# Optimization experiments

Measured on AMD Instinct MI355X. Metric: run time of the kernel, lower is better.

## Reference

```python
import jax, jax.numpy as jnp
import numpy as np

N, M, E, IN, HID = 100000, 2048, 65536, 512, 256
TAU, LAMDA = 0.5, 1.0


def _l2n(a, eps=1e-12):
    # F.normalize: x / max(||x||_2, eps) along dim=1
    return a / jnp.maximum(jnp.linalg.norm(a, axis=1, keepdims=True), eps)


def setup_inputs() -> dict:
    key = jax.random.key(0)
    ks = jax.random.split(key, 16)
    s = 0.05  # weight scale (xavier-like)
    inp = {
        "x": jax.random.normal(ks[0], (N, IN), jnp.float32),
        "We0": jax.random.normal(ks[1], (IN, HID), jnp.float32) * s,
        "be0": jnp.zeros((HID,), jnp.float32),
        "We1": jax.random.normal(ks[2], (HID, HID), jnp.float32) * s,
        "be1": jnp.zeros((HID,), jnp.float32),
        "Wt0": jax.random.normal(ks[3], (IN, HID), jnp.float32) * s,
        "bt0": jnp.zeros((HID,), jnp.float32),
        "Wt1": jax.random.normal(ks[4], (HID, HID), jnp.float32) * s,
        "bt1": jnp.zeros((HID,), jnp.float32),
        "Wp0": jax.random.normal(ks[5], (HID, HID), jnp.float32) * s,
        "bp0": jnp.zeros((HID,), jnp.float32),
        "Wp1": jax.random.normal(ks[6], (HID, HID), jnp.float32) * s,
        "bp1": jnp.zeros((HID,), jnp.float32),
        "p_vals": jnp.ones((N,), jnp.float32),
        "cg_vals": jax.random.uniform(ks[7], (E,), jnp.float32),
        "p_assign": jax.random.randint(ks[8], (N,), 0, M, jnp.int32),
        "cg_rows": jax.random.randint(ks[9], (E,), 0, M, jnp.int32),
        "cg_cols": jax.random.randint(ks[10], (E,), 0, M, jnp.int32),
        "neg_idx": jax.random.randint(ks[11], (N,), 0, M, jnp.int32),
    }
    return inp


def reference(x, We0, be0, We1, be1, Wt0, bt0, Wt1, bt1,
              Wp0, bp0, Wp1, bp1, p_vals, cg_vals,
              p_assign, cg_rows, cg_cols, neg_idx):
    # encoder: stacked Linears, no activation (batch_norm=layer_norm=False)
    h = (x @ We0 + be0) @ We1 + be1                      # [N, HID]
    # h = spmm(P.T, h): per-cluster weighted sum
    hc = jax.ops.segment_sum(p_vals[:, None] * h, p_assign, num_segments=M)  # [M, HID]
    # target encoder
    v = (x @ Wt0 + bt0) @ Wt1 + bt1                      # [N, HID]

    # pos_score: projector (relu between layers, none on last) + normalize
    q = jax.nn.relu(hc @ Wp0 + bp0) @ Wp1 + bp1          # [M, HID]
    q = _l2n(q)
    vn = _l2n(v)
    pos_sim = jnp.sum(vn * q[p_assign], axis=1) / TAU    # [N]
    pos_score = jnp.exp(
        jax.ops.segment_sum(p_vals * pos_sim, p_assign, num_segments=M))[:, None]  # [M,1]

    # neg_score: dense cluster-cluster similarity
    hn = _l2n(hc)
    neg_score = jnp.exp((hn @ hn.T) / TAU)               # [M, M]

    # partition_score = coarse_g @ neg_score (sparse row-scatter)
    partition_score = jax.ops.segment_sum(
        cg_vals[:, None] * neg_score[cg_cols], cg_rows, num_segments=M)  # [M, M]

    loss = jnp.mean(-jnp.log(pos_score + LAMDA * partition_score)
                    + jnp.log(pos_score + neg_score.sum(axis=1)))
    return loss
```

## Files before the change

kernel.cpp:

```cpp
#include <hip/hip_runtime.h>
#include <hip/hip_bf16.h>
#include <math.h>

#define N_PTS  100000
#define M_CL   2048
#define E_EDG  65536
#define IN_DIM 512
#define HID    256

typedef unsigned short u16;
typedef __attribute__((ext_vector_type(8))) short bf16x8;
typedef __attribute__((ext_vector_type(4))) float f32x4;

__device__ __forceinline__ u16 f2bf(float f){
  __hip_bfloat16 h = __float2bfloat16(f);
  return *reinterpret_cast<u16*>(&h);
}
__device__ __forceinline__ unsigned pk2(float a, float b){
  return (unsigned)f2bf(a) | ((unsigned)f2bf(b) << 16);
}
__device__ __forceinline__ float bf2f(u16 v){
  return __uint_as_float((unsigned)v << 16);
}
__device__ __forceinline__ void glds16(const u16* g, u16* lds_base_uniform){
  __builtin_amdgcn_global_load_lds(
      (const __attribute__((address_space(1))) unsigned int*)(g),
      (__attribute__((address_space(3))) unsigned int*)(lds_base_uniform), 16, 0, 0);
}
#define VMWAIT8() do{ asm volatile("s_waitcnt vmcnt(8)" ::: "memory"); __builtin_amdgcn_sched_barrier(0);}while(0)
#define VMWAIT4() do{ asm volatile("s_waitcnt vmcnt(4)" ::: "memory"); __builtin_amdgcn_sched_barrier(0);}while(0)
#define VMWAIT0() do{ asm volatile("s_waitcnt vmcnt(0)" ::: "memory"); __builtin_amdgcn_sched_barrier(0);}while(0)

static const size_t OFF_POSACC = 0;
static const size_t OFF_NEGSUM = 8192;
static const size_t OFF_HISTP  = 16384;
static const size_t OFF_CURP   = 24576;
static const size_t OFF_HISTE  = 32768;
static const size_t OFF_CURE   = 40960;
static const size_t OFF_LOSS   = 49152;
static const size_t ZERO_BYTES = 49408;
static const size_t OFF_STARTP = 49664;
static const size_t OFF_STARTE = 58112;
static const size_t OFF_SORTPT = 66560;
static const size_t OFF_SCOL   = 466688;
static const size_t OFF_SVAL   = 728832;
static const size_t OFF_CNT    = 990976;
static const size_t OFF_XC     = 999168;
static const size_t OFF_Q      = 9387776;
static const size_t OFF_HNB    = 11484928;
static const size_t OFF_NEGB   = 13582080;
static const size_t OFF_WT0T   = 22020096;
static const size_t OFF_WT1T   = 22282240;
static const size_t OFF_XBF    = 33554432;

__global__ __launch_bounds__(256) void k_zero(unsigned* __restrict__ p, int n){
  int i = blockIdx.x*256 + threadIdx.x;
  if (i < n) p[i] = 0u;
}

__global__ __launch_bounds__(256) void k_hist(const int* __restrict__ idx, int n, int* __restrict__ hist){
  int i = blockIdx.x*256 + threadIdx.x;
  if (i < n) atomicAdd(&hist[idx[i]], 1);
}

__global__ __launch_bounds__(256) void k_scan(const int* __restrict__ hist, int* __restrict__ start){
  __shared__ int part[256];
  int t = threadIdx.x;
  int v[8]; int s = 0;
#pragma unroll
  for (int j=0;j<8;j++){ v[j] = hist[t*8+j]; s += v[j]; }
  part[t] = s;
  __syncthreads();
  if (t == 0){
    int run = 0;
    for (int i=0;i<256;i++){ int tmp = part[i]; part[i] = run; run += tmp; }
  }
  __syncthreads();
  int run = part[t];
#pragma unroll
  for (int j=0;j<8;j++){ start[t*8+j] = run; run += v[j]; }
  if (t == 255) start[M_CL] = run;
}

__global__ __launch_bounds__(256) void k_scatter_pts(const int* __restrict__ assign, const int* __restrict__ start,
                                                     int* __restrict__ cur, int* __restrict__ out){
  int i = blockIdx.x*256 + threadIdx.x;
  if (i < N_PTS){
    int r = assign[i];
    int p = start[r] + atomicAdd(&cur[r], 1);
    out[p] = i;
  }
}

__global__ __launch_bounds__(256) void k_scatter_edges(const int* __restrict__ rows, const int* __restrict__ cols,
                                                       const float* __restrict__ vals, const int* __restrict__ start,
                                                       int* __restrict__ cur, int* __restrict__ scol,
                                                       float* __restrict__ sval){
  int e = blockIdx.x*256 + threadIdx.x;
  if (e < E_EDG){
    int r = rows[e];
    int p = start[r] + atomicAdd(&cur[r], 1);
    scol[p] = cols[e];
    sval[p] = vals[e];
  }
}

__global__ __launch_bounds__(256) void k_cluster_agg(const float* __restrict__ x, const float* __restrict__ pv,
                                                     const int* __restrict__ sorted_pt, const int* __restrict__ start,
                                                     float* __restrict__ Xc, float* __restrict__ cnt,
                                                     u16* __restrict__ xbf){
  const int m = blockIdx.x;
  const int t = threadIdx.x;
  const int half = t >> 7;
  const int u = t & 127;
  const int s0 = start[m], s1 = start[m+1];
  f32x4 a = {0.f,0.f,0.f,0.f};
  float c = 0.f;
  for (int p = s0 + half; p < s1; p += 2){
    int row = sorted_pt[p];
    float w = pv[row];
    f32x4 xv = *reinterpret_cast<const f32x4*>(x + (size_t)row*IN_DIM + u*4);
    a.x = fmaf(w, xv.x, a.x); a.y = fmaf(w, xv.y, a.y);
    a.z = fmaf(w, xv.z, a.z); a.w = fmaf(w, xv.w, a.w);
    c += w;
    uint2 pk; pk.x = pk2(xv.x, xv.y); pk.y = pk2(xv.z, xv.w);
    *reinterpret_cast<uint2*>(xbf + (size_t)row*IN_DIM + u*4) = pk;
  }
  __shared__ __align__(16) float sh[128*4];
  __shared__ float shc[2];
  if (half == 1) *reinterpret_cast<f32x4*>(sh + u*4) = a;
  if (t == 0)   shc[0] = c;
  if (t == 128) shc[1] = c;
  __syncthreads();
  if (half == 0){
    f32x4 b = *reinterpret_cast<const f32x4*>(sh + u*4);
    a.x += b.x; a.y += b.y; a.z += b.z; a.w += b.w;
    *reinterpret_cast<f32x4*>(Xc + (size_t)m*IN_DIM + u*4) = a;
    if (t == 0) cnt[m] = shc[0] + shc[1];
  }
}

template<int K>
__global__ __launch_bounds__(256) void k_transpose_bf16(const float* __restrict__ W, u16* __restrict__ Wt){
  int o = blockIdx.x*256 + threadIdx.x;
  int n = o / K, k = o % K;
  Wt[o] = f2bf(W[(size_t)k*HID + n]);
}

template<int K>
__device__ __forceinline__ void mc_layer(const float* __restrict__ W, const float* act, int t, float acc[4]){
#pragma unroll
  for (int r=0;r<4;r++) acc[r] = 0.f;
#pragma unroll 2
  for (int k=0;k<K;k+=4){
    float w0 = W[(size_t)(k+0)*HID + t];
    float w1 = W[(size_t)(k+1)*HID + t];
    float w2 = W[(size_t)(k+2)*HID + t];
    float w3 = W[(size_t)(k+3)*HID + t];
#pragma unroll
    for (int r=0;r<4;r++){
      float4 av = *reinterpret_cast<const float4*>(act + r*K + k);
      acc[r] = fmaf(av.x, w0, acc[r]);
      acc[r] = fmaf(av.y, w1, acc[r]);
      acc[r] = fmaf(av.z, w2, acc[r]);
      acc[r] = fmaf(av.w, w3, acc[r]);
    }
  }
}

__global__ __launch_bounds__(256) void k_mchain(
    const float* __restrict__ Xc, const float* __restrict__ cnt,
    const float* __restrict__ We0, const float* __restrict__ be0,
    const float* __restrict__ We1, const float* __restrict__ be1,
    const float* __restrict__ Wp0, const float* __restrict__ bp0,
    const float* __restrict__ Wp1, const float* __restrict__ bp1,
    u16* __restrict__ hnb, float* __restrict__ q){
  __shared__ __align__(16) float a_sh[4*512];
  __shared__ __align__(16) float b_sh[4*256];
  __shared__ float part[4][4];
  const int t = threadIdx.x;
  const int rb = blockIdx.x*4;
  for (int i=t; i<4*128; i+=256){
    int r = i>>7, k4 = i&127;
    reinterpret_cast<float4*>(a_sh + r*512)[k4] =
      reinterpret_cast<const float4*>(Xc + (size_t)(rb+r)*IN_DIM)[k4];
  }
  float cv[4];
#pragma unroll
  for (int r=0;r<4;r++) cv[r] = cnt[rb+r];
  __syncthreads();

  float acc[4], v[4];
  mc_layer<512>(We0, a_sh, t, acc);
  {
    float b = be0[t];
#pragma unroll
    for (int r=0;r<4;r++) b_sh[r*256+t] = fmaf(cv[r], b, acc[r]);
  }
  __syncthreads();
  mc_layer<256>(We1, b_sh, t, acc);
  {
    float b = be1[t];
#pragma unroll
    for (int r=0;r<4;r++){
      v[r] = fmaf(cv[r], b, acc[r]);
      float s = v[r]*v[r];
#pragma unroll
      for (int off=32;off;off>>=1) s += __shfl_xor(s, off, 64);
      if ((t&63) == 0) part[t>>6][r] = s;
      a_sh[r*256+t] = v[r];
    }
  }
  __syncthreads();
#pragma unroll
  for (int r=0;r<4;r++){
    float tot = part[0][r]+part[1][r]+part[2][r]+part[3][r];
    float inv = 1.0f / fmaxf(sqrtf(tot), 1e-12f);
    hnb[(size_t)(rb+r)*HID + t] = f2bf(v[r]*inv);
  }
  mc_layer<256>(Wp0, a_sh, t, acc);
  {
    float b = bp0[t];
#pragma unroll
    for (int r=0;r<4;r++) b_sh[r*256+t] = fmaxf(acc[r]+b, 0.f);
  }
  __syncthreads();
  mc_layer<256>(Wp1, b_sh, t, acc);
  {
    float b = bp1[t];
#pragma unroll
    for (int r=0;r<4;r++){
      v[r] = acc[r] + b;
      float s = v[r]*v[r];
#pragma unroll
      for (int off=32;off;off>>=1) s += __shfl_xor(s, off, 64);
      if ((t&63) == 0) part[t>>6][r] = s;
    }
  }
  __syncthreads();
#pragma unroll
  for (int r=0;r<4;r++){
    float tot = part[0][r]+part[1][r]+part[2][r]+part[3][r];
    float inv = 1.0f / fmaxf(sqrtf(tot), 1e-12f);
    q[(size_t)(rb+r)*HID + t] = v[r]*inv;
  }
}

__global__ __launch_bounds__(256,2) void k_target_mfma(
    const u16* __restrict__ xbf, const u16* __restrict__ Wt0t, const float* __restrict__ bt0,
    const u16* __restrict__ Wt1t, const float* __restrict__ bt1,
    const float* __restrict__ q, const int* __restrict__ assign,
    const float* __restrict__ pv, float* __restrict__ posacc){
  __shared__ u16 wlds[4][2][2048];
  __shared__ u16 act[16384];
  __shared__ float red[2][4][4][16];

  const int t  = threadIdx.x;
  const int w  = t >> 6;
  const int l  = t & 63;
  const int c  = l & 15;
  const int lg = l >> 4;
  const int gm0 = blockIdx.x * 64;

  const int wrow = l >> 2;
  const int wswz = (l&3) ^ ((wrow>>1)&3);

  #define TSTAGE_W(Wt, K, k0, buf) do { \
    _Pragma("unroll") \
    for (int i_=0;i_<4;i_++){ \
      int row_ = w*64 + i_*16 + wrow; \
      glds16((Wt) + (size_t)row_*(K) + (k0) + wswz*8, &wlds[w][buf][i_*512]); \
    } } while(0)

  const u16* xrow[4];
#pragma unroll
  for (int mf=0;mf<4;mf++){
    int gm = gm0 + mf*16 + c; if (gm > N_PTS-1) gm = N_PTS-1;
    xrow[mf] = xbf + (size_t)gm*IN_DIM + lg*8;
  }

  f32x4 acc[4][4];
#pragma unroll
  for (int i=0;i<4;i++)
#pragma unroll
    for (int j=0;j<4;j++){ acc[i][j].x=0.f; acc[i][j].y=0.f; acc[i][j].z=0.f; acc[i][j].w=0.f; }

  const int su = lg ^ ((c>>1)&3);

  bf16x8 xreg[2][4];
  TSTAGE_W(Wt0t, IN_DIM, 0, 0);
#pragma unroll
  for (int mf=0;mf<4;mf++) xreg[0][mf] = *reinterpret_cast<const bf16x8*>(xrow[mf]);

#pragma unroll
  for (int ks=0; ks<16; ks++){
    const int buf = ks & 1;
    if (ks < 15){
      TSTAGE_W(Wt0t, IN_DIM, (ks+1)*32, buf^1);
#pragma unroll
      for (int mf=0;mf<4;mf++)
        xreg[buf^1][mf] = *reinterpret_cast<const bf16x8*>(xrow[mf] + (ks+1)*32);
      VMWAIT8();
    } else {
      VMWAIT0();
    }
#pragma unroll
    for (int nf=0; nf<4; nf++){
      bf16x8 afr = *reinterpret_cast<const bf16x8*>(&wlds[w][buf][((nf*16+c)*4 + su)*8]);
#pragma unroll
      for (int mf=0; mf<4; mf++)
        acc[mf][nf] = __builtin_amdgcn_mfma_f32_16x16x32_bf16(afr, xreg[buf][mf], acc[mf][nf], 0,0,0);
    }
  }

#pragma unroll
  for (int nf=0; nf<4; nf++){
    f32x4 bias = *reinterpret_cast<const f32x4*>(bt0 + w*64 + nf*16 + lg*4);
#pragma unroll
    for (int mf=0; mf<4; mf++){
      int m = mf*16 + c;
      f32x4 v = acc[mf][nf] + bias;
      uint2 p; p.x = pk2(v.x, v.y); p.y = pk2(v.z, v.w);
      int u = (w*8 + nf*2 + (lg>>1)) ^ (c&7);
      *reinterpret_cast<uint2*>(act + (m*32 + u)*8 + (lg&1)*4) = p;
    }
  }
#pragma unroll
  for (int i=0;i<4;i++)
#pragma unroll
    for (int j=0;j<4;j++){ acc[i][j].x=0.f; acc[i][j].y=0.f; acc[i][j].z=0.f; acc[i][j].w=0.f; }
  __syncthreads();

  TSTAGE_W(Wt1t, HID, 0, 0);
#pragma unroll
  for (int ks=0; ks<8; ks++){
    const int buf = ks & 1;
    if (ks < 7){
      TSTAGE_W(Wt1t, HID, (ks+1)*32, buf^1);
      VMWAIT4();
    } else {
      VMWAIT0();
    }
    bf16x8 bfr[4];
#pragma unroll
    for (int mf=0; mf<4; mf++){
      int m = mf*16 + c;
      int u = (ks*4 + lg) ^ (c&7);
      bfr[mf] = *reinterpret_cast<const bf16x8*>(act + (m*32 + u)*8);
    }
#pragma unroll
    for (int nf=0; nf<4; nf++){
      bf16x8 afr = *reinterpret_cast<const bf16x8*>(&wlds[w][buf][((nf*16+c)*4 + su)*8]);
#pragma unroll
      for (int mf=0; mf<4; mf++)
        acc[mf][nf] = __builtin_amdgcn_mfma_f32_16x16x32_bf16(afr, bfr[mf], acc[mf][nf], 0,0,0);
    }
  }

#pragma unroll
  for (int mf=0; mf<4; mf++){
    int gm = gm0 + mf*16 + c;
    int cl = assign[(gm < N_PTS) ? gm : (N_PTS-1)];
    const float* qrow = q + (size_t)cl*HID + w*64 + lg*4;
    float ss = 0.f, d = 0.f;
#pragma unroll
    for (int nf=0; nf<4; nf++){
      f32x4 b  = *reinterpret_cast<const f32x4*>(bt1 + w*64 + nf*16 + lg*4);
      f32x4 qv = *reinterpret_cast<const f32x4*>(qrow + nf*16);
      f32x4 v  = acc[mf][nf] + b;
      ss = fmaf(v.x,v.x, fmaf(v.y,v.y, fmaf(v.z,v.z, fmaf(v.w,v.w, ss))));
      d  = fmaf(v.x,qv.x, fmaf(v.y,qv.y, fmaf(v.z,qv.z, fmaf(v.w,qv.w, d))));
    }
    ss += __shfl_xor(ss, 16, 64); ss += __shfl_xor(ss, 32, 64);
    d  += __shfl_xor(d , 16, 64); d  += __shfl_xor(d , 32, 64);
    if (lg == 0){ red[0][w][mf][c] = ss; red[1][w][mf][c] = d; }
  }
  __syncthreads();
  if (t < 64){
    int gm = gm0 + t;
    if (gm < N_PTS){
      int mf = t>>4, cc = t&15;
      float ss = red[0][0][mf][cc]+red[0][1][mf][cc]+red[0][2][mf][cc]+red[0][3][mf][cc];
      float d  = red[1][0][mf][cc]+red[1][1][mf][cc]+red[1][2][mf][cc]+red[1][3][mf][cc];
      float inv = 1.0f / fmaxf(sqrtf(ss), 1e-12f);
      atomicAdd(&posacc[assign[gm]], pv[gm] * d * inv * 2.0f);
    }
  }
  #undef TSTAGE_W
}

__global__ __launch_bounds__(256) void k_neg_mfma(
    const u16* __restrict__ hnb, u16* __restrict__ negb, float* __restrict__ negsum){
  __shared__ u16 wlds[4][2][2048];
  const int t  = threadIdx.x;
  const int w  = t >> 6;
  const int l  = t & 63;
  const int c  = l & 15;
  const int lg = l >> 4;
  const int j0 = blockIdx.x * 256;
  const int i0 = blockIdx.y * 64;

  const int wrow = l >> 2;
  const int wswz = (l&3) ^ ((wrow>>1)&3);

  #define NSTAGE_W(k0, buf) do { \
    _Pragma("unroll") \
    for (int i_=0;i_<4;i_++){ \
      int row_ = j0 + w*64 + i_*16 + wrow; \
      glds16(hnb + (size_t)row_*HID + (k0) + wswz*8, &wlds[w][buf][i_*512]); \
    } } while(0)

  const u16* irow[4];
#pragma unroll
  for (int mf=0;mf<4;mf++)
    irow[mf] = hnb + (size_t)(i0 + mf*16 + c)*HID + lg*8;

  f32x4 acc[4][4];
#pragma unroll
  for (int i=0;i<4;i++)
#pragma unroll
    for (int j=0;j<4;j++){ acc[i][j].x=0.f; acc[i][j].y=0.f; acc[i][j].z=0.f; acc[i][j].w=0.f; }

  const int su = lg ^ ((c>>1)&3);

  bf16x8 xreg[2][4];
  NSTAGE_W(0, 0);
#pragma unroll
  for (int mf=0;mf<4;mf++) xreg[0][mf] = *reinterpret_cast<const bf16x8*>(irow[mf]);

#pragma unroll
  for (int ks=0; ks<8; ks++){
    const int buf = ks & 1;
    if (ks < 7){
      NSTAGE_W((ks+1)*32, buf^1);
#pragma unroll
      for (int mf=0;mf<4;mf++)
        xreg[buf^1][mf] = *reinterpret_cast<const bf16x8*>(irow[mf] + (ks+1)*32);
      VMWAIT8();
    } else {
      VMWAIT0();
    }
#pragma unroll
    for (int nf=0; nf<4; nf++){
      bf16x8 afr = *reinterpret_cast<const bf16x8*>(&wlds[w][buf][((nf*16+c)*4 + su)*8]);
#pragma unroll
      for (int mf=0; mf<4; mf++)
        acc[mf][nf] = __builtin_amdgcn_mfma_f32_16x16x32_bf16(afr, xreg[buf][mf], acc[mf][nf], 0,0,0);
    }
  }

#pragma unroll
  for (int mf=0; mf<4; mf++){
    int i = i0 + mf*16 + c;
    float rs = 0.f;
#pragma unroll
    for (int nf=0; nf<4; nf++){
      f32x4 a = acc[mf][nf];
      float e0 = __expf(a.x*2.0f), e1 = __expf(a.y*2.0f);
      float e2 = __expf(a.z*2.0f), e3 = __expf(a.w*2.0f);
      rs += e0+e1+e2+e3;
      uint2 p; p.x = pk2(e0, e1); p.y = pk2(e2, e3);
      *reinterpret_cast<uint2*>(negb + (size_t)i*M_CL + j0 + w*64 + nf*16 + lg*4) = p;
    }
    rs += __shfl_xor(rs, 16, 64); rs += __shfl_xor(rs, 32, 64);
    if (lg == 0) atomicAdd(&negsum[i], rs);
  }
  #undef NSTAGE_W
}

__global__ __launch_bounds__(256) void k_loss(const u16* __restrict__ negb, const float* __restrict__ negsum,
                                              const float* __restrict__ posacc, const int* __restrict__ start,
                                              const int* __restrict__ scol, const float* __restrict__ sval,
                                              double* __restrict__ loss){
  const int i = blockIdx.x, t = threadIdx.x;
  float ps[8] = {};
  const int s0 = start[i], s1 = start[i+1];
  for (int e=s0;e<s1;e++){
    int c = scol[e];
    float v = sval[e];
    bf16x8 r = *reinterpret_cast<const bf16x8*>(negb + (size_t)c*M_CL + t*8);
#pragma unroll
    for (int jj=0;jj<8;jj++) ps[jj] = fmaf(v, bf2f((u16)r[jj]), ps[jj]);
  }
  float pos = __expf(posacc[i]);
  f32x4 nsa = *reinterpret_cast<const f32x4*>(negsum + t*8);
  f32x4 nsb = *reinterpret_cast<const f32x4*>(negsum + t*8 + 4);
  float ns[8] = {nsa.x,nsa.y,nsa.z,nsa.w,nsb.x,nsb.y,nsb.z,nsb.w};
  float part = 0.f;
#pragma unroll
  for (int jj=0;jj<8;jj++)
    part += __logf(pos + ns[jj]) - __logf(pos + ps[jj]);
#pragma unroll
  for (int off=32;off;off>>=1) part += __shfl_xor(part, off, 64);
  __shared__ float wsum[4];
  if ((t&63) == 0) wsum[t>>6] = part;
  __syncthreads();
  if (t == 0){
    double s = (double)wsum[0] + (double)wsum[1] + (double)wsum[2] + (double)wsum[3];
    atomicAdd(loss, s);
  }
}

__global__ void k_finalize(const double* __restrict__ loss, float* __restrict__ out){
  if (threadIdx.x == 0 && blockIdx.x == 0)
    out[0] = (float)(loss[0] / ((double)M_CL * (double)M_CL));
}

extern "C" void kernel_launch(void* const* d_in, const int* in_sizes, int n_in,
                              void* d_out, int out_size, void* d_ws, size_t ws_size,
                              hipStream_t stream){
  const float* x    = (const float*)d_in[0];
  const float* We0  = (const float*)d_in[1];
  const float* be0  = (const float*)d_in[2];
  const float* We1  = (const float*)d_in[3];
  const float* be1  = (const float*)d_in[4];
  const float* Wt0  = (const float*)d_in[5];
  const float* bt0  = (const float*)d_in[6];
  const float* Wt1  = (const float*)d_in[7];
  const float* bt1  = (const float*)d_in[8];
  const float* Wp0  = (const float*)d_in[9];
  const float* bp0  = (const float*)d_in[10];
  const float* Wp1  = (const float*)d_in[11];
  const float* bp1  = (const float*)d_in[12];
  const float* pv   = (const float*)d_in[13];
  const float* cgv  = (const float*)d_in[14];
  const int*   pas  = (const int*)d_in[15];
  const int*   cgr  = (const int*)d_in[16];
  const int*   cgc  = (const int*)d_in[17];

  char* ws = (char*)d_ws;
  float*  posacc  = (float*)(ws + OFF_POSACC);
  float*  negsum  = (float*)(ws + OFF_NEGSUM);
  int*    hist_p  = (int*)  (ws + OFF_HISTP);
  int*    cur_p   = (int*)  (ws + OFF_CURP);
  int*    hist_e  = (int*)  (ws + OFF_HISTE);
  int*    cur_e   = (int*)  (ws + OFF_CURE);
  double* lossd   = (double*)(ws + OFF_LOSS);
  int*    start_p = (int*)  (ws + OFF_STARTP);
  int*    start_e = (int*)  (ws + OFF_STARTE);
  int*    sortpt  = (int*)  (ws + OFF_SORTPT);
  int*    scol    = (int*)  (ws + OFF_SCOL);
  float*  sval    = (float*)(ws + OFF_SVAL);
  float*  cnt     = (float*)(ws + OFF_CNT);
  float*  Xc      = (float*)(ws + OFF_XC);
  float*  qb      = (float*)(ws + OFF_Q);
  u16*    hnb     = (u16*)  (ws + OFF_HNB);
  u16*    negb    = (u16*)  (ws + OFF_NEGB);
  u16*    Wt0t    = (u16*)  (ws + OFF_WT0T);
  u16*    Wt1t    = (u16*)  (ws + OFF_WT1T);
  u16*    xbf     = (u16*)  (ws + OFF_XBF);

  k_zero<<<(ZERO_BYTES/4 + 255)/256, 256, 0, stream>>>((unsigned*)ws, ZERO_BYTES/4);

  k_hist<<<(N_PTS+255)/256, 256, 0, stream>>>(pas, N_PTS, hist_p);
  k_hist<<<(E_EDG+255)/256, 256, 0, stream>>>(cgr, E_EDG, hist_e);
  k_scan<<<1, 256, 0, stream>>>(hist_p, start_p);
  k_scan<<<1, 256, 0, stream>>>(hist_e, start_e);
  k_scatter_pts<<<(N_PTS+255)/256, 256, 0, stream>>>(pas, start_p, cur_p, sortpt);
  k_scatter_edges<<<(E_EDG+255)/256, 256, 0, stream>>>(cgr, cgc, cgv, start_e, cur_e, scol, sval);

  k_transpose_bf16<IN_DIM><<<IN_DIM, 256, 0, stream>>>(Wt0, Wt0t);
  k_transpose_bf16<HID  ><<<HID,    256, 0, stream>>>(Wt1, Wt1t);

  k_cluster_agg<<<M_CL, 256, 0, stream>>>(x, pv, sortpt, start_p, Xc, cnt, xbf);

  k_mchain<<<M_CL/4, 256, 0, stream>>>(Xc, cnt, We0, be0, We1, be1, Wp0, bp0, Wp1, bp1, hnb, qb);

  k_target_mfma<<<(N_PTS+63)/64, 256, 0, stream>>>(xbf, Wt0t, bt0, Wt1t, bt1, qb, pas, pv, posacc);

  dim3 gneg(M_CL/256, M_CL/64);
  k_neg_mfma<<<gneg, 256, 0, stream>>>(hnb, negb, negsum);

  k_loss<<<M_CL, 256, 0, stream>>>(negb, negsum, posacc, start_e, scol, sval, lossd);
  k_finalize<<<1, 64, 0, stream>>>(lossd, (float*)d_out);
}
```

Baseline: 360.1 us.

## Merge setup, scatter, transpose and neg/target GEMM kernels to cut launches

Replaces the zero, histogram, scan, scatter and transpose launches with a single-block setup kernel (LDS histograms and wave scans) plus one multi-role scatter/transpose kernel. Merges the neg-similarity GEMM and the target-encoder GEMM into one launch split by block index, so the two run concurrently. Folds the finalize step into the loss kernel through a last-block ticket counter. This removes several kernel launches and their serialization gaps. In exchange, the histograms now run serially in one 1024-thread block, and the merged kernel's occupancy and register limits now apply to both roles.

```diff
diff --git a/kernel.cpp b/kernel.cpp
--- a/kernel.cpp
+++ b/kernel.cpp
@@ -33,75 +33,111 @@
 
 static const size_t OFF_POSACC = 0;
 static const size_t OFF_NEGSUM = 8192;
-static const size_t OFF_HISTP  = 16384;
-static const size_t OFF_CURP   = 24576;
-static const size_t OFF_HISTE  = 32768;
-static const size_t OFF_CURE   = 40960;
-static const size_t OFF_LOSS   = 49152;
-static const size_t ZERO_BYTES = 49408;
-static const size_t OFF_STARTP = 49664;
-static const size_t OFF_STARTE = 58112;
-static const size_t OFF_SORTPT = 66560;
-static const size_t OFF_SCOL   = 466688;
-static const size_t OFF_SVAL   = 728832;
-static const size_t OFF_CNT    = 990976;
-static const size_t OFF_XC     = 999168;
-static const size_t OFF_Q      = 9387776;
-static const size_t OFF_HNB    = 11484928;
-static const size_t OFF_NEGB   = 13582080;
+static const size_t OFF_CURP   = 16384;
+static const size_t OFF_CURE   = 24576;
+static const size_t OFF_LOSS   = 32768;
+static const size_t OFF_DONE   = 32776;
+static const size_t OFF_STARTP = 33024;
+static const size_t OFF_STARTE = 41472;
+static const size_t OFF_SORTPT = 49920;
+static const size_t OFF_SCOL   = 450048;
+static const size_t OFF_SVAL   = 712192;
+static const size_t OFF_CNT    = 974336;
+static const size_t OFF_XC     = 982528;
+static const size_t OFF_Q      = 9371136;
+static const size_t OFF_HNB    = 11468288;
+static const size_t OFF_NEGB   = 13565440;
 static const size_t OFF_WT0T   = 22020096;
 static const size_t OFF_WT1T   = 22282240;
 static const size_t OFF_XBF    = 33554432;
 
-__global__ __launch_bounds__(256) void k_zero(unsigned* __restrict__ p, int n){
-  int i = blockIdx.x*256 + threadIdx.x;
-  if (i < n) p[i] = 0u;
-}
-
-__global__ __launch_bounds__(256) void k_hist(const int* __restrict__ idx, int n, int* __restrict__ hist){
-  int i = blockIdx.x*256 + threadIdx.x;
-  if (i < n) atomicAdd(&hist[idx[i]], 1);
-}
-
-__global__ __launch_bounds__(256) void k_scan(const int* __restrict__ hist, int* __restrict__ start){
-  __shared__ int part[256];
-  int t = threadIdx.x;
-  int v[8]; int s = 0;
-#pragma unroll
-  for (int j=0;j<8;j++){ v[j] = hist[t*8+j]; s += v[j]; }
-  part[t] = s;
-  __syncthreads();
-  if (t == 0){
-    int run = 0;
-    for (int i=0;i<256;i++){ int tmp = part[i]; part[i] = run; run += tmp; }
-  }
-  __syncthreads();
-  int run = part[t];
-#pragma unroll
-  for (int j=0;j<8;j++){ start[t*8+j] = run; run += v[j]; }
-  if (t == 255) start[M_CL] = run;
-}
-
-__global__ __launch_bounds__(256) void k_scatter_pts(const int* __restrict__ assign, const int* __restrict__ start,
-                                                     int* __restrict__ cur, int* __restrict__ out){
-  int i = blockIdx.x*256 + threadIdx.x;
-  if (i < N_PTS){
-    int r = assign[i];
-    int p = start[r] + atomicAdd(&cur[r], 1);
-    out[p] = i;
-  }
-}
-
-__global__ __launch_bounds__(256) void k_scatter_edges(const int* __restrict__ rows, const int* __restrict__ cols,
-                                                       const float* __restrict__ vals, const int* __restrict__ start,
-                                                       int* __restrict__ cur, int* __restrict__ scol,
-                                                       float* __restrict__ sval){
-  int e = blockIdx.x*256 + threadIdx.x;
-  if (e < E_EDG){
-    int r = rows[e];
-    int p = start[r] + atomicAdd(&cur[r], 1);
-    scol[p] = cols[e];
-    sval[p] = vals[e];
+__global__ __launch_bounds__(1024) void k_setup(
+    const int* __restrict__ pas, const int* __restrict__ cgr,
+    int* __restrict__ start_p, int* __restrict__ start_e,
+    int* __restrict__ cur_p, int* __restrict__ cur_e,
+    float* __restrict__ posacc, float* __restrict__ negsum,
+    double* __restrict__ lossd, int* __restrict__ done){
+  __shared__ int hist[2048];
+  __shared__ int wpart[16];
+  const int t = threadIdx.x;
+  const int lane = t & 63, wv = t >> 6;
+
+  posacc[2*t] = 0.f; posacc[2*t+1] = 0.f;
+  negsum[2*t] = 0.f; negsum[2*t+1] = 0.f;
+  cur_p[2*t] = 0;    cur_p[2*t+1] = 0;
+  cur_e[2*t] = 0;    cur_e[2*t+1] = 0;
+  if (t == 0){ *lossd = 0.0; *done = 0; }
+  hist[2*t] = 0; hist[2*t+1] = 0;
+  __syncthreads();
+
+  for (int i=t; i<N_PTS; i+=1024) atomicAdd(&hist[pas[i]], 1);
+  __syncthreads();
+  {
+    int v0 = hist[2*t], v1 = hist[2*t+1];
+    int s = v0 + v1;
+    for (int off=1; off<64; off<<=1){ int n = __shfl_up(s, off, 64); if (lane >= off) s += n; }
+    if (lane == 63) wpart[wv] = s;
+    __syncthreads();
+    if (t == 0){ int run = 0; for (int i=0;i<16;i++){ int tmp = wpart[i]; wpart[i] = run; run += tmp; } }
+    __syncthreads();
+    int excl = s - (v0+v1) + wpart[wv];
+    start_p[2*t] = excl; start_p[2*t+1] = excl + v0;
+    if (t == 1023) start_p[2048] = excl + v0 + v1;
+  }
+  __syncthreads();
+  hist[2*t] = 0; hist[2*t+1] = 0;
+  __syncthreads();
+  for (int i=t; i<E_EDG; i+=1024) atomicAdd(&hist[cgr[i]], 1);
+  __syncthreads();
+  {
+    int v0 = hist[2*t], v1 = hist[2*t+1];
+    int s = v0 + v1;
+    for (int off=1; off<64; off<<=1){ int n = __shfl_up(s, off, 64); if (lane >= off) s += n; }
+    if (lane == 63) wpart[wv] = s;
+    __syncthreads();
+    if (t == 0){ int run = 0; for (int i=0;i<16;i++){ int tmp = wpart[i]; wpart[i] = run; run += tmp; } }
+    __syncthreads();
+    int excl = s - (v0+v1) + wpart[wv];
+    start_e[2*t] = excl; start_e[2*t+1] = excl + v0;
+    if (t == 1023) start_e[2048] = excl + v0 + v1;
+  }
+}
+
+#define NB_P  ((N_PTS + 255)/256)
+#define NB_E  ((E_EDG + 255)/256)
+#define NB_T0 ((256*512)/256)
+#define NB_T1 ((256*256)/256)
+__global__ __launch_bounds__(256) void k_misc(
+    const int* __restrict__ pas, const int* __restrict__ cgr, const int* __restrict__ cgc,
+    const float* __restrict__ cgv, const int* __restrict__ start_p, const int* __restrict__ start_e,
+    int* __restrict__ cur_p, int* __restrict__ cur_e,
+    int* __restrict__ sortpt, int* __restrict__ scol, float* __restrict__ sval,
+    const float* __restrict__ Wt0, const float* __restrict__ Wt1,
+    u16* __restrict__ Wt0t, u16* __restrict__ Wt1t){
+  const int b = blockIdx.x, t = threadIdx.x;
+  if (b < NB_P){
+    int i = b*256 + t;
+    if (i < N_PTS){
+      int r = pas[i];
+      int p = start_p[r] + atomicAdd(&cur_p[r], 1);
+      sortpt[p] = i;
+    }
+  } else if (b < NB_P + NB_E){
+    int e = (b - NB_P)*256 + t;
+    if (e < E_EDG){
+      int r = cgr[e];
+      int p = start_e[r] + atomicAdd(&cur_e[r], 1);
+      scol[p] = cgc[e];
+      sval[p] = cgv[e];
+    }
+  } else if (b < NB_P + NB_E + NB_T0){
+    int o = (b - NB_P - NB_E)*256 + t;
+    int n = o / IN_DIM, k = o % IN_DIM;
+    Wt0t[o] = f2bf(Wt0[(size_t)k*HID + n]);
+  } else {
+    int o = (b - NB_P - NB_E - NB_T0)*256 + t;
+    int n = o / HID, k = o % HID;
+    Wt1t[o] = f2bf(Wt1[(size_t)k*HID + n]);
   }
 }
 
@@ -141,13 +177,6 @@
 }
 
 template<int K>
-__global__ __launch_bounds__(256) void k_transpose_bf16(const float* __restrict__ W, u16* __restrict__ Wt){
-  int o = blockIdx.x*256 + threadIdx.x;
-  int n = o / K, k = o % K;
-  Wt[o] = f2bf(W[(size_t)k*HID + n]);
-}
-
-template<int K>
 __device__ __forceinline__ void mc_layer(const float* __restrict__ W, const float* act, int t, float acc[4]){
 #pragma unroll
   for (int r=0;r<4;r++) acc[r] = 0.f;
@@ -246,11 +275,14 @@
   }
 }
 
-__global__ __launch_bounds__(256,2) void k_target_mfma(
+#define NEG_BLKS 256
+#define TGT_BLKS ((N_PTS + 63)/64)
+__global__ __launch_bounds__(256,2) void k_tneg(
     const u16* __restrict__ xbf, const u16* __restrict__ Wt0t, const float* __restrict__ bt0,
     const u16* __restrict__ Wt1t, const float* __restrict__ bt1,
     const float* __restrict__ q, const int* __restrict__ assign,
-    const float* __restrict__ pv, float* __restrict__ posacc){
+    const float* __restrict__ pv, float* __restrict__ posacc,
+    const u16* __restrict__ hnb, u16* __restrict__ negb, float* __restrict__ negsum){
   __shared__ u16 wlds[4][2][2048];
   __shared__ u16 act[16384];
   __shared__ float red[2][4][4][16];
@@ -260,10 +292,80 @@
   const int l  = t & 63;
   const int c  = l & 15;
   const int lg = l >> 4;
-  const int gm0 = blockIdx.x * 64;
-
   const int wrow = l >> 2;
   const int wswz = (l&3) ^ ((wrow>>1)&3);
+  const int su = lg ^ ((c>>1)&3);
+
+  f32x4 acc[4][4];
+#pragma unroll
+  for (int i=0;i<4;i++)
+#pragma unroll
+    for (int j=0;j<4;j++){ acc[i][j].x=0.f; acc[i][j].y=0.f; acc[i][j].z=0.f; acc[i][j].w=0.f; }
+
+  if (blockIdx.x < NEG_BLKS){
+    const int b  = blockIdx.x;
+    const int j0 = (b & 7) * 256;
+    const int i0 = (b >> 3) * 64;
+
+    #define NSTAGE_W(k0, buf) do { \
+      _Pragma("unroll") \
+      for (int i_=0;i_<4;i_++){ \
+        int row_ = j0 + w*64 + i_*16 + wrow; \
+        glds16(hnb + (size_t)row_*HID + (k0) + wswz*8, &wlds[w][buf][i_*512]); \
+      } } while(0)
+
+    const u16* irow[4];
+#pragma unroll
+    for (int mf=0;mf<4;mf++)
+      irow[mf] = hnb + (size_t)(i0 + mf*16 + c)*HID + lg*8;
+
+    bf16x8 xreg[2][4];
+    NSTAGE_W(0, 0);
+#pragma unroll
+    for (int mf=0;mf<4;mf++) xreg[0][mf] = *reinterpret_cast<const bf16x8*>(irow[mf]);
+
+#pragma unroll
+    for (int ks=0; ks<8; ks++){
+      const int buf = ks & 1;
+      if (ks < 7){
+        NSTAGE_W((ks+1)*32, buf^1);
+#pragma unroll
+        for (int mf=0;mf<4;mf++)
+          xreg[buf^1][mf] = *reinterpret_cast<const bf16x8*>(irow[mf] + (ks+1)*32);
+        VMWAIT8();
+      } else {
+        VMWAIT0();
+      }
+#pragma unroll
+      for (int nf=0; nf<4; nf++){
+        bf16x8 afr = *reinterpret_cast<const bf16x8*>(&wlds[w][buf][((nf*16+c)*4 + su)*8]);
+#pragma unroll
+        for (int mf=0; mf<4; mf++)
+          acc[mf][nf] = __builtin_amdgcn_mfma_f32_16x16x32_bf16(afr, xreg[buf][mf], acc[mf][nf], 0,0,0);
+      }
+    }
+
+#pragma unroll
+    for (int mf=0; mf<4; mf++){
+      int i = i0 + mf*16 + c;
+      float rs = 0.f;
+#pragma unroll
+      for (int nf=0; nf<4; nf++){
+        f32x4 a = acc[mf][nf];
+        float e0 = __expf(a.x*2.0f), e1 = __expf(a.y*2.0f);
+        float e2 = __expf(a.z*2.0f), e3 = __expf(a.w*2.0f);
+        rs += e0+e1+e2+e3;
+        uint2 p; p.x = pk2(e0, e1); p.y = pk2(e2, e3);
+        *reinterpret_cast<uint2*>(negb + (size_t)i*M_CL + j0 + w*64 + nf*16 + lg*4) = p;
+      }
+      rs += __shfl_xor(rs, 16, 64); rs += __shfl_xor(rs, 32, 64);
+      if (lg == 0) atomicAdd(&negsum[i], rs);
+    }
+    #undef NSTAGE_W
+    return;
+  }
+
+  const int gm0 = (blockIdx.x - NEG_BLKS) * 64;
 
   #define TSTAGE_W(Wt, K, k0, buf) do { \
     _Pragma("unroll") \
@@ -278,14 +380,6 @@
     int gm = gm0 + mf*16 + c; if (gm > N_PTS-1) gm = N_PTS-1;
     xrow[mf] = xbf + (size_t)gm*IN_DIM + lg*8;
   }
-
-  f32x4 acc[4][4];
-#pragma unroll
-  for (int i=0;i<4;i++)
-#pragma unroll
-    for (int j=0;j<4;j++){ acc[i][j].x=0.f; acc[i][j].y=0.f; acc[i][j].z=0.f; acc[i][j].w=0.f; }
-
-  const int su = lg ^ ((c>>1)&3);
 
   bf16x8 xreg[2][4];
   TSTAGE_W(Wt0t, IN_DIM, 0, 0);
@@ -389,89 +483,11 @@
   #undef TSTAGE_W
 }
 
-__global__ __launch_bounds__(256) void k_neg_mfma(
-    const u16* __restrict__ hnb, u16* __restrict__ negb, float* __restrict__ negsum){
-  __shared__ u16 wlds[4][2][2048];
-  const int t  = threadIdx.x;
-  const int w  = t >> 6;
-  const int l  = t & 63;
-  const int c  = l & 15;
-  const int lg = l >> 4;
-  const int j0 = blockIdx.x * 256;
-  const int i0 = blockIdx.y * 64;
-
-  const int wrow = l >> 2;
-  const int wswz = (l&3) ^ ((wrow>>1)&3);
-
-  #define NSTAGE_W(k0, buf) do { \
-    _Pragma("unroll") \
-    for (int i_=0;i_<4;i_++){ \
-      int row_ = j0 + w*64 + i_*16 + wrow; \
-      glds16(hnb + (size_t)row_*HID + (k0) + wswz*8, &wlds[w][buf][i_*512]); \
-    } } while(0)
-
-  const u16* irow[4];
-#pragma unroll
-  for (int mf=0;mf<4;mf++)
-    irow[mf] = hnb + (size_t)(i0 + mf*16 + c)*HID + lg*8;
-
-  f32x4 acc[4][4];
-#pragma unroll
-  for (int i=0;i<4;i++)
-#pragma unroll
-    for (int j=0;j<4;j++){ acc[i][j].x=0.f; acc[i][j].y=0.f; acc[i][j].z=0.f; acc[i][j].w=0.f; }
-
-  const int su = lg ^ ((c>>1)&3);
-
-  bf16x8 xreg[2][4];
-  NSTAGE_W(0, 0);
-#pragma unroll
-  for (int mf=0;mf<4;mf++) xreg[0][mf] = *reinterpret_cast<const bf16x8*>(irow[mf]);
-
-#pragma unroll
-  for (int ks=0; ks<8; ks++){
-    const int buf = ks & 1;
-    if (ks < 7){
-      NSTAGE_W((ks+1)*32, buf^1);
-#pragma unroll
-      for (int mf=0;mf<4;mf++)
-        xreg[buf^1][mf] = *reinterpret_cast<const bf16x8*>(irow[mf] + (ks+1)*32);
-      VMWAIT8();
-    } else {
-      VMWAIT0();
-    }
-#pragma unroll
-    for (int nf=0; nf<4; nf++){
-      bf16x8 afr = *reinterpret_cast<const bf16x8*>(&wlds[w][buf][((nf*16+c)*4 + su)*8]);
-#pragma unroll
-      for (int mf=0; mf<4; mf++)
-        acc[mf][nf] = __builtin_amdgcn_mfma_f32_16x16x32_bf16(afr, xreg[buf][mf], acc[mf][nf], 0,0,0);
-    }
-  }
-
-#pragma unroll
-  for (int mf=0; mf<4; mf++){
-    int i = i0 + mf*16 + c;
-    float rs = 0.f;
-#pragma unroll
-    for (int nf=0; nf<4; nf++){
-      f32x4 a = acc[mf][nf];
-      float e0 = __expf(a.x*2.0f), e1 = __expf(a.y*2.0f);
-      float e2 = __expf(a.z*2.0f), e3 = __expf(a.w*2.0f);
-      rs += e0+e1+e2+e3;
-      uint2 p; p.x = pk2(e0, e1); p.y = pk2(e2, e3);
-      *reinterpret_cast<uint2*>(negb + (size_t)i*M_CL + j0 + w*64 + nf*16 + lg*4) = p;
-    }
-    rs += __shfl_xor(rs, 16, 64); rs += __shfl_xor(rs, 32, 64);
-    if (lg == 0) atomicAdd(&negsum[i], rs);
-  }
-  #undef NSTAGE_W
-}
-
 __global__ __launch_bounds__(256) void k_loss(const u16* __restrict__ negb, const float* __restrict__ negsum,
                                               const float* __restrict__ posacc, const int* __restrict__ start,
                                               const int* __restrict__ scol, const float* __restrict__ sval,
-                                              double* __restrict__ loss){
+                                              double* __restrict__ lossd, int* __restrict__ done,
+                                              float* __restrict__ out){
   const int i = blockIdx.x, t = threadIdx.x;
   float ps[8] = {};
   const int s0 = start[i], s1 = start[i+1];
@@ -497,13 +513,15 @@
   __syncthreads();
   if (t == 0){
     double s = (double)wsum[0] + (double)wsum[1] + (double)wsum[2] + (double)wsum[3];
-    atomicAdd(loss, s);
-  }
-}
-
-__global__ void k_finalize(const double* __restrict__ loss, float* __restrict__ out){
-  if (threadIdx.x == 0 && blockIdx.x == 0)
-    out[0] = (float)(loss[0] / ((double)M_CL * (double)M_CL));
+    atomicAdd(lossd, s);
+    __threadfence();
+    int ticket = atomicAdd(done, 1);
+    if (ticket == M_CL - 1){
+      __threadfence();
+      double tot = atomicAdd(lossd, 0.0);
+      out[0] = (float)(tot / ((double)M_CL * (double)M_CL));
+    }
+  }
 }
 
 extern "C" void kernel_launch(void* const* d_in, const int* in_sizes, int n_in,
@@ -531,11 +549,10 @@
   char* ws = (char*)d_ws;
   float*  posacc  = (float*)(ws + OFF_POSACC);
   float*  negsum  = (float*)(ws + OFF_NEGSUM);
-  int*    hist_p  = (int*)  (ws + OFF_HISTP);
   int*    cur_p   = (int*)  (ws + OFF_CURP);
-  int*    hist_e  = (int*)  (ws + OFF_HISTE);
   int*    cur_e   = (int*)  (ws + OFF_CURE);
   double* lossd   = (double*)(ws + OFF_LOSS);
+  int*    done    = (int*)  (ws + OFF_DONE);
   int*    start_p = (int*)  (ws + OFF_STARTP);
   int*    start_e = (int*)  (ws + OFF_STARTE);
   int*    sortpt  = (int*)  (ws + OFF_SORTPT);
@@ -550,27 +567,19 @@
   u16*    Wt1t    = (u16*)  (ws + OFF_WT1T);
   u16*    xbf     = (u16*)  (ws + OFF_XBF);
 
-  k_zero<<<(ZERO_BYTES/4 + 255)/256, 256, 0, stream>>>((unsigned*)ws, ZERO_BYTES/4);
-
-  k_hist<<<(N_PTS+255)/256, 256, 0, stream>>>(pas, N_PTS, hist_p);
-  k_hist<<<(E_EDG+255)/256, 256, 0, stream>>>(cgr, E_EDG, hist_e);
-  k_scan<<<1, 256, 0, stream>>>(hist_p, start_p);
-  k_scan<<<1, 256, 0, stream>>>(hist_e, start_e);
-  k_scatter_pts<<<(N_PTS+255)/256, 256, 0, stream>>>(pas, start_p, cur_p, sortpt);
-  k_scatter_edges<<<(E_EDG+255)/256, 256, 0, stream>>>(cgr, cgc, cgv, start_e, cur_e, scol, sval);
-
-  k_transpose_bf16<IN_DIM><<<IN_DIM, 256, 0, stream>>>(Wt0, Wt0t);
-  k_transpose_bf16<HID  ><<<HID,    256, 0, stream>>>(Wt1, Wt1t);
+  k_setup<<<1, 1024, 0, stream>>>(pas, cgr, start_p, start_e, cur_p, cur_e,
+                                  posacc, negsum, lossd, done);
+
+  k_misc<<<NB_P + NB_E + NB_T0 + NB_T1, 256, 0, stream>>>(
+      pas, cgr, cgc, cgv, start_p, start_e, cur_p, cur_e,
+      sortpt, scol, sval, Wt0, Wt1, Wt0t, Wt1t);
 
   k_cluster_agg<<<M_CL, 256, 0, stream>>>(x, pv, sortpt, start_p, Xc, cnt, xbf);
 
   k_mchain<<<M_CL/4, 256, 0, stream>>>(Xc, cnt, We0, be0, We1, be1, Wp0, bp0, Wp1, bp1, hnb, qb);
 
-  k_target_mfma<<<(N_PTS+63)/64, 256, 0, stream>>>(xbf, Wt0t, bt0, Wt1t, bt1, qb, pas, pv, posacc);
-
-  dim3 gneg(M_CL/256, M_CL/64);
-  k_neg_mfma<<<gneg, 256, 0, stream>>>(hnb, negb, negsum);
-
-  k_loss<<<M_CL, 256, 0, stream>>>(negb, negsum, posacc, start_e, scol, sval, lossd);
-  k_finalize<<<1, 64, 0, stream>>>(lossd, (float*)d_out);
-}
+  k_tneg<<<NEG_BLKS + TGT_BLKS, 256, 0, stream>>>(
+      xbf, Wt0t, bt0, Wt1t, bt1, qb, pas, pv, posacc, hnb, negb, negsum);
+
+  k_loss<<<M_CL, 256, 0, stream>>>(negb, negsum, posacc, start_e, scol, sval, lossd, done, (float*)d_out);
+}
```

After: 397.9 us. 10.5% more time.
